# Optimization experiments

Measured on AMD Instinct MI355X. Metric: run time of the kernel, lower is better.

## Reference

```python
import jax, jax.numpy as jnp
import numpy as np

B, T = 64, 512          # batch, input_size
VOCAB = 16              # Embedding(16, ...)
UNITS = 256             # embedding dim
H = 512                 # LSTM hidden units (hard-coded in module)
F = 64                  # num_features (dense output)


def _glorot(key, shape):
    lim = np.sqrt(6.0 / (shape[0] + shape[1]))
    return jax.random.uniform(key, shape, jnp.float32, -lim, lim)


def setup_inputs() -> dict:
    key = jax.random.key(0)
    ks = jax.random.split(key, 9)
    tokens = jax.random.randint(ks[0], (B, T), 0, VOCAB, dtype=jnp.int32)
    return {
        "tokens": tokens,
        "emb": _glorot(ks[1], (VOCAB, UNITS)),
        "W1": _glorot(ks[2], (UNITS, 4 * H)),
        "U1": _glorot(ks[3], (H, 4 * H)),
        "b1": jnp.zeros((4 * H,), jnp.float32),
        "W2": _glorot(ks[4], (H, 4 * H)),
        "U2": _glorot(ks[5], (H, 4 * H)),
        "b2": jnp.zeros((4 * H,), jnp.float32),
        "Wd": _glorot(ks[6], (H, F)),
        "bd": jnp.zeros((F,), jnp.float32),
    }


def _lstm(x, mask, W, U, b, return_sequences):
    # x: [B, T, D]; mask: [B, T] bool. Keras semantics: masked steps carry
    # previous h and c (state and output pass through unchanged).
    xT = jnp.swapaxes(x, 0, 1)      # [T, B, D]
    mT = jnp.swapaxes(mask, 0, 1)   # [T, B]
    h0 = jnp.zeros((x.shape[0], U.shape[0]), x.dtype)
    c0 = h0

    def step(carry, inp):
        h, c = carry
        xt, mt = inp
        z = xt @ W + h @ U + b                    # [B, 4H]
        i, f, g, o = jnp.split(z, 4, axis=-1)     # Keras gate order i,f,c,o
        i = jax.nn.sigmoid(i)
        f = jax.nn.sigmoid(f)
        o = jax.nn.sigmoid(o)
        c_new = f * c + i * jnp.tanh(g)
        h_new = o * jnp.tanh(c_new)
        m = mt[:, None]
        h_new = jnp.where(m, h_new, h)
        c_new = jnp.where(m, c_new, c)
        return (h_new, c_new), h_new

    (h_last, _), hs = jax.lax.scan(step, (h0, c0), (xT, mT))
    return jnp.swapaxes(hs, 0, 1) if return_sequences else h_last


def reference(tokens, emb, W1, U1, b1, W2, U2, b2, Wd, bd):
    mask = tokens != 0                 # mask_zero=True
    x = emb[tokens]                    # [B, T, UNITS]
    h1 = _lstm(x, mask, W1, U1, b1, return_sequences=True)   # [B, T, H]
    h2 = _lstm(h1, mask, W2, U2, b2, return_sequences=False)  # [B, H]
    return h2 @ Wd + bd                # [B, F]
```

## Files before the change

### kernel.cpp

```cpp
#include <hip/hip_runtime.h>

#define BB   64
#define TT   512
#define NVOC 16
#define KIN  256
#define HH   512
#define GG   2048
#define FF   64

#define NWG  256
#define NTHR 512

#define U1W_OFF  0
#define W2W_OFF  8384
#define U2W_OFF  16768
#define HLDS_OFF 25152
#define ZRED_OFF 33344
#define TABW_OFF 37696
#define B2W_OFF  37952
#define LDS_FLOATS 37968
#define LDS_BYTES  (LDS_FLOATS * 4)

#define H1A_OFF 0
#define H1B_OFF 32768
#define H2A_OFF 65536
#define H2B_OFF 98304

__device__ __forceinline__ void wg_barrier(unsigned* ctr, unsigned target) {
  __syncthreads();
  if (threadIdx.x == 0) {
    __hip_atomic_fetch_add(ctr, 1u, __ATOMIC_RELEASE, __HIP_MEMORY_SCOPE_AGENT);
    while (__hip_atomic_load(ctr, __ATOMIC_ACQUIRE, __HIP_MEMORY_SCOPE_AGENT) < target) {
      __builtin_amdgcn_s_sleep(2);
    }
  }
  __syncthreads();
}

__device__ __forceinline__ void stage_ld(float4 v[4], const float* __restrict__ src, int tid) {
  #pragma unroll
  for (int jj = 0; jj < 4; ++jj) {
    int f4 = jj * 512 + tid;
    int b = f4 >> 6, k4l = f4 & 63;
    v[jj] = *reinterpret_cast<const float4*>(src + b * HH + k4l * 4);
  }
}
__device__ __forceinline__ void stage_st(float* __restrict__ hlds, const float4 v[4], int tid) {
  float4* h4 = reinterpret_cast<float4*>(hlds);
  #pragma unroll
  for (int jj = 0; jj < 4; ++jj) {
    int f4 = jj * 512 + tid;
    int b = f4 >> 6, k4l = f4 & 63;
    h4[b * 64 + (k4l ^ (b >> 3))] = v[jj];
  }
}

__device__ __forceinline__ void inner8(float acc[8], const float* __restrict__ wrow,
                                       const float4* __restrict__ h4base, int kq8, int bg) {
  #pragma unroll
  for (int j = 0; j < 8; ++j) {
    int k4 = kq8 + j;
    float4 w = *reinterpret_cast<const float4*>(wrow + k4 * 4);
    const float4* hb = h4base + (k4 ^ bg);
    float4 h0 = hb[0 * 64], h1 = hb[1 * 64], h2 = hb[2 * 64], h3 = hb[3 * 64];
    float4 h4v = hb[4 * 64], h5 = hb[5 * 64], h6 = hb[6 * 64], h7 = hb[7 * 64];
    acc[0] += h0.x * w.x; acc[0] += h0.y * w.y; acc[0] += h0.z * w.z; acc[0] += h0.w * w.w;
    acc[1] += h1.x * w.x; acc[1] += h1.y * w.y; acc[1] += h1.z * w.z; acc[1] += h1.w * w.w;
    acc[2] += h2.x * w.x; acc[2] += h2.y * w.y; acc[2] += h2.z * w.z; acc[2] += h2.w * w.w;
    acc[3] += h3.x * w.x; acc[3] += h3.y * w.y; acc[3] += h3.z * w.z; acc[3] += h3.w * w.w;
    acc[4] += h4v.x * w.x; acc[4] += h4v.y * w.y; acc[4] += h4v.z * w.z; acc[4] += h4v.w * w.w;
    acc[5] += h5.x * w.x; acc[5] += h5.y * w.y; acc[5] += h5.z * w.z; acc[5] += h5.w * w.w;
    acc[6] += h6.x * w.x; acc[6] += h6.y * w.y; acc[6] += h6.z * w.z; acc[6] += h6.w * w.w;
    acc[7] += h7.x * w.x; acc[7] += h7.y * w.y; acc[7] += h7.z * w.z; acc[7] += h7.w * w.w;
  }
}

extern "C" __global__ void __launch_bounds__(NTHR, 2)
lstm_fused2(const int* __restrict__ tokens, const float* __restrict__ emb,
            const float* __restrict__ W1, const float* __restrict__ U1,
            const float* __restrict__ b1, const float* __restrict__ W2,
            const float* __restrict__ U2, const float* __restrict__ b2,
            const float* __restrict__ Wd, const float* __restrict__ bd,
            float* __restrict__ out, float* __restrict__ wsf,
            unsigned* __restrict__ ctr)
{
  extern __shared__ float lds[];
  float* u1w  = lds + U1W_OFF;
  float* w2w  = lds + W2W_OFF;
  float* u2w  = lds + U2W_OFF;
  float* hlds = lds + HLDS_OFF;
  float* zred = lds + ZRED_OFF;
  float* tabw = lds + TABW_OFF;
  float* b2w  = lds + B2W_OFF;

  const int wg  = blockIdx.x;
  const int tid = threadIdx.x;
  const int bh  = wg >> 7;
  const int ct  = wg & 127;
  const int hc0 = ct * 4;
  const int zcl = tid & 15;
  const int bg  = (tid >> 4) & 3;
  const int kq  = tid >> 6;
  const int kq8 = kq * 8;

  float* h1A = wsf + H1A_OFF; float* h1B = wsf + H1B_OFF;
  float* h2A = wsf + H2A_OFF; float* h2B = wsf + H2B_OFF;

  {
    int k = tid;
    #pragma unroll
    for (int g = 0; g < 4; ++g) {
      float4 a = *reinterpret_cast<const float4*>(U1 + (size_t)k * GG + hc0 + 512 * g);
      u1w[(g * 4 + 0) * 524 + k] = a.x; u1w[(g * 4 + 1) * 524 + k] = a.y;
      u1w[(g * 4 + 2) * 524 + k] = a.z; u1w[(g * 4 + 3) * 524 + k] = a.w;
      float4 b_ = *reinterpret_cast<const float4*>(W2 + (size_t)k * GG + hc0 + 512 * g);
      w2w[(g * 4 + 0) * 524 + k] = b_.x; w2w[(g * 4 + 1) * 524 + k] = b_.y;
      w2w[(g * 4 + 2) * 524 + k] = b_.z; w2w[(g * 4 + 3) * 524 + k] = b_.w;
      float4 c_ = *reinterpret_cast<const float4*>(U2 + (size_t)k * GG + hc0 + 512 * g);
      u2w[(g * 4 + 0) * 524 + k] = c_.x; u2w[(g * 4 + 1) * 524 + k] = c_.y;
      u2w[(g * 4 + 2) * 524 + k] = c_.z; u2w[(g * 4 + 3) * 524 + k] = c_.w;
    }
  }
  if (tid < 256) {
    int v = tid >> 4, zz = tid & 15;
    int col = hc0 + (zz & 3) + ((zz >> 2) << 9);
    float a = b1[col];
    #pragma unroll 4
    for (int k = 0; k < KIN; ++k) a += emb[v * KIN + k] * W1[(size_t)k * GG + col];
    tabw[v * 16 + zz] = a;
  }
  if (tid < 16) b2w[tid] = b2[hc0 + (tid & 3) + ((tid >> 2) << 9)];
  {
    if (tid < 128)       h1A[bh * 16384 + ct * 128 + tid] = 0.f;
    else if (tid < 256)  h2A[bh * 16384 + ct * 128 + (tid - 128)] = 0.f;
  }
  unsigned bt = 128;
  wg_barrier(&ctr[bh], bt);

  float c1 = 0.f, hp1 = 0.f, c2 = 0.f, hp2 = 0.f;
  const int fb = tid >> 2;
  const int fc = tid & 3;

  const float4* h4base = reinterpret_cast<const float4*>(hlds) + bg * 512;
  const float* u1row = u1w + zcl * 524;
  const float* w2row = w2w + zcl * 524;
  const float* u2row = u2w + zcl * 524;

  for (int t = 0; t < TT; ++t) {
    float* h1r = (t & 1) ? h1B : h1A;
    float* h1w = (t & 1) ? h1A : h1B;
    float* h2r = (t & 1) ? h2B : h2A;
    float* h2w = (t & 1) ? h2A : h2B;
    const float* h1r_half = h1r + bh * 32 * HH;
    const float* h2r_half = h2r + bh * 32 * HH;
    const float* h1w_half = h1w + bh * 32 * HH;

    float acc[8] = {0,0,0,0,0,0,0,0};
    float4 pre[4];

    stage_ld(pre, h1r_half, tid);
    __syncthreads(); stage_st(hlds, pre, tid); __syncthreads();
    stage_ld(pre, h1r_half + 256, tid);
    inner8(acc, u1row, h4base, kq8, bg);
    __syncthreads(); stage_st(hlds, pre, tid); __syncthreads();
    stage_ld(pre, h2r_half, tid);
    inner8(acc, u1row + 256, h4base, kq8, bg);

    __syncthreads();
    #pragma unroll
    for (int i = 0; i < 8; ++i) zred[kq * 544 + (bg * 8 + i) * 17 + zcl] = acc[i];
    __syncthreads();
    if (tid < 128) {
      float z[4];
      #pragma unroll
      for (int g = 0; g < 4; ++g) {
        float s = 0.f;
        #pragma unroll
        for (int q = 0; q < 8; ++q) s += zred[q * 544 + fb * 17 + g * 4 + fc];
        z[g] = s;
      }
      int tok = tokens[(bh * 32 + fb) * TT + t];
      #pragma unroll
      for (int g = 0; g < 4; ++g) z[g] += tabw[tok * 16 + g * 4 + fc];
      float si = 1.f / (1.f + expf(-z[0]));
      float sf = 1.f / (1.f + expf(-z[1]));
      float gg = tanhf(z[2]);
      float so = 1.f / (1.f + expf(-z[3]));
      float cn = sf * c1 + si * gg;
      float hn = so * tanhf(cn);
      if (tok == 0) { cn = c1; hn = hp1; }
      c1 = cn; hp1 = hn;
      h1w[(bh * 32 + fb) * HH + hc0 + fc] = hn;
    }
    bt += 128; wg_barrier(&ctr[bh], bt);

    #pragma unroll
    for (int i = 0; i < 8; ++i) acc[i] = 0.f;
    __syncthreads(); stage_st(hlds, pre, tid); __syncthreads();
    stage_ld(pre, h2r_half + 256, tid);
    inner8(acc, u2row, h4base, kq8, bg);
    __syncthreads(); stage_st(hlds, pre, tid); __syncthreads();
    stage_ld(pre, h1w_half, tid);
    inner8(acc, u2row + 256, h4base, kq8, bg);
    __syncthreads(); stage_st(hlds, pre, tid); __syncthreads();
    stage_ld(pre, h1w_half + 256, tid);
    inner8(acc, w2row, h4base, kq8, bg);
    __syncthreads(); stage_st(hlds, pre, tid); __syncthreads();
    inner8(acc, w2row + 256, h4base, kq8, bg);

    __syncthreads();
    #pragma unroll
    for (int i = 0; i < 8; ++i) zred[kq * 544 + (bg * 8 + i) * 17 + zcl] = acc[i];
    __syncthreads();
    if (tid < 128) {
      float z[4];
      #pragma unroll
      for (int g = 0; g < 4; ++g) {
        float s = 0.f;
        #pragma unroll
        for (int q = 0; q < 8; ++q) s += zred[q * 544 + fb * 17 + g * 4 + fc];
        z[g] = s + b2w[g * 4 + fc];
      }
      int tok = tokens[(bh * 32 + fb) * TT + t];
      float si = 1.f / (1.f + expf(-z[0]));
      float sf = 1.f / (1.f + expf(-z[1]));
      float gg = tanhf(z[2]);
      float so = 1.f / (1.f + expf(-z[3]));
      float cn = sf * c2 + si * gg;
      float hn = so * tanhf(cn);
      if (tok == 0) { cn = c2; hn = hp2; }
      c2 = cn; hp2 = hn;
      h2w[(bh * 32 + fb) * HH + hc0 + fc] = hn;
    }
    bt += 128; wg_barrier(&ctr[bh], bt);
  }

  if (ct < 4) {
    int idx = ct * 512 + tid;
    int b = idx >> 6, f = idx & 63;
    const float* hf = h2A + (bh * 32 + b) * HH;
    float a = bd[f];
    #pragma unroll 8
    for (int k = 0; k < HH; ++k) a += hf[k] * Wd[(size_t)k * FF + f];
    out[(bh * 32 + b) * FF + f] = a;
  }
}

extern "C" void kernel_launch(void* const* d_in, const int* in_sizes, int n_in,
                              void* d_out, int out_size, void* d_ws, size_t ws_size,
                              hipStream_t stream) {
  const int*   tokens = (const int*)  d_in[0];
  const float* emb    = (const float*)d_in[1];
  const float* W1     = (const float*)d_in[2];
  const float* U1     = (const float*)d_in[3];
  const float* b1     = (const float*)d_in[4];
  const float* W2     = (const float*)d_in[5];
  const float* U2     = (const float*)d_in[6];
  const float* b2     = (const float*)d_in[7];
  const float* Wd     = (const float*)d_in[8];
  const float* bd     = (const float*)d_in[9];
  float*    out = (float*)d_out;
  unsigned* ctr = (unsigned*)d_ws;
  float*    wsf = (float*)((char*)d_ws + 64);

  hipFuncSetAttribute((const void*)lstm_fused2,
                      hipFuncAttributeMaxDynamicSharedMemorySize, LDS_BYTES);

  hipMemsetAsync(d_ws, 0, 64, stream);

  void* args[] = { &tokens, &emb, &W1, &U1, &b1, &W2, &U2, &b2, &Wd, &bd,
                   &out, &wsf, &ctr };
  hipLaunchCooperativeKernel((void*)lstm_fused2, dim3(NWG), dim3(NTHR),
                             args, LDS_BYTES, stream);
}
```

Baseline: 28.02 ms.

## Replace atomic counter barriers with per-workgroup flags and split layer waits

```diff
diff --git a/kernel.cpp b/kernel.cpp
--- a/kernel.cpp
+++ b/kernel.cpp
@@ -21,18 +21,23 @@
 #define LDS_FLOATS 37968
 #define LDS_BYTES  (LDS_FLOATS * 4)
 
+#define FLAG_WORDS 8192
 #define H1A_OFF 0
 #define H1B_OFF 32768
 #define H2A_OFF 65536
 #define H2B_OFF 98304
 
-__device__ __forceinline__ void wg_barrier(unsigned* ctr, unsigned target) {
+__device__ __forceinline__ void bar_arrive(unsigned* flag, unsigned val) {
   __syncthreads();
-  if (threadIdx.x == 0) {
-    __hip_atomic_fetch_add(ctr, 1u, __ATOMIC_RELEASE, __HIP_MEMORY_SCOPE_AGENT);
-    while (__hip_atomic_load(ctr, __ATOMIC_ACQUIRE, __HIP_MEMORY_SCOPE_AGENT) < target) {
-      __builtin_amdgcn_s_sleep(2);
-    }
+  if (threadIdx.x == 0)
+    __hip_atomic_store(flag, val, __ATOMIC_RELEASE, __HIP_MEMORY_SCOPE_AGENT);
+}
+
+__device__ __forceinline__ void bar_wait(unsigned* flags, unsigned target) {
+  if (threadIdx.x < 128) {
+    unsigned* f = flags + threadIdx.x * 16;
+    while (__hip_atomic_load(f, __ATOMIC_ACQUIRE, __HIP_MEMORY_SCOPE_AGENT) < target)
+      __builtin_amdgcn_s_sleep(4);
   }
   __syncthreads();
 }
@@ -76,13 +81,13 @@
 }
 
 extern "C" __global__ void __launch_bounds__(NTHR, 2)
-lstm_fused2(const int* __restrict__ tokens, const float* __restrict__ emb,
+lstm_fused3(const int* __restrict__ tokens, const float* __restrict__ emb,
             const float* __restrict__ W1, const float* __restrict__ U1,
             const float* __restrict__ b1, const float* __restrict__ W2,
             const float* __restrict__ U2, const float* __restrict__ b2,
             const float* __restrict__ Wd, const float* __restrict__ bd,
             float* __restrict__ out, float* __restrict__ wsf,
-            unsigned* __restrict__ ctr)
+            unsigned* __restrict__ flags)
 {
   extern __shared__ float lds[];
   float* u1w  = lds + U1W_OFF;
@@ -102,6 +107,11 @@
   const int bg  = (tid >> 4) & 3;
   const int kq  = tid >> 6;
   const int kq8 = kq * 8;
+
+  unsigned* fA = flags + bh * 2048;
+  unsigned* fB = flags + 4096 + bh * 2048;
+  unsigned* myA = fA + ct * 16;
+  unsigned* myB = fB + ct * 16;
 
   float* h1A = wsf + H1A_OFF; float* h1B = wsf + H1B_OFF;
   float* h2A = wsf + H2A_OFF; float* h2B = wsf + H2B_OFF;
@@ -134,8 +144,9 @@
     if (tid < 128)       h1A[bh * 16384 + ct * 128 + tid] = 0.f;
     else if (tid < 256)  h2A[bh * 16384 + ct * 128 + (tid - 128)] = 0.f;
   }
-  unsigned bt = 128;
-  wg_barrier(&ctr[bh], bt);
+  bar_arrive(myA, 1u);
+  bar_arrive(myB, 1u);
+  bar_wait(fA, 1u);
 
   float c1 = 0.f, hp1 = 0.f, c2 = 0.f, hp2 = 0.f;
   const int fb = tid >> 2;
@@ -154,6 +165,7 @@
     const float* h1r_half = h1r + bh * 32 * HH;
     const float* h2r_half = h2r + bh * 32 * HH;
     const float* h1w_half = h1w + bh * 32 * HH;
+    const unsigned stamp = (unsigned)t + 2u;
 
     float acc[8] = {0,0,0,0,0,0,0,0};
     float4 pre[4];
@@ -163,7 +175,6 @@
     stage_ld(pre, h1r_half + 256, tid);
     inner8(acc, u1row, h4base, kq8, bg);
     __syncthreads(); stage_st(hlds, pre, tid); __syncthreads();
-    stage_ld(pre, h2r_half, tid);
     inner8(acc, u1row + 256, h4base, kq8, bg);
 
     __syncthreads();
@@ -192,16 +203,20 @@
       c1 = cn; hp1 = hn;
       h1w[(bh * 32 + fb) * HH + hc0 + fc] = hn;
     }
-    bt += 128; wg_barrier(&ctr[bh], bt);
-
+    bar_arrive(myA, stamp);
+
+    bar_wait(fB, stamp - 1u);
     #pragma unroll
     for (int i = 0; i < 8; ++i) acc[i] = 0.f;
+    stage_ld(pre, h2r_half, tid);
     __syncthreads(); stage_st(hlds, pre, tid); __syncthreads();
     stage_ld(pre, h2r_half + 256, tid);
     inner8(acc, u2row, h4base, kq8, bg);
     __syncthreads(); stage_st(hlds, pre, tid); __syncthreads();
+    inner8(acc, u2row + 256, h4base, kq8, bg);
+
+    bar_wait(fA, stamp);
     stage_ld(pre, h1w_half, tid);
-    inner8(acc, u2row + 256, h4base, kq8, bg);
     __syncthreads(); stage_st(hlds, pre, tid); __syncthreads();
     stage_ld(pre, h1w_half + 256, tid);
     inner8(acc, w2row, h4base, kq8, bg);
@@ -232,9 +247,10 @@
       c2 = cn; hp2 = hn;
       h2w[(bh * 32 + fb) * HH + hc0 + fc] = hn;
     }
-    bt += 128; wg_barrier(&ctr[bh], bt);
-  }
-
+    bar_arrive(myB, stamp);
+  }
+
+  bar_wait(fB, (unsigned)TT + 1u);
   if (ct < 4) {
     int idx = ct * 512 + tid;
     int b = idx >> 6, f = idx & 63;
@@ -259,17 +275,17 @@
   const float* b2     = (const float*)d_in[7];
   const float* Wd     = (const float*)d_in[8];
   const float* bd     = (const float*)d_in[9];
-  float*    out = (float*)d_out;
-  unsigned* ctr = (unsigned*)d_ws;
-  float*    wsf = (float*)((char*)d_ws + 64);
-
-  hipFuncSetAttribute((const void*)lstm_fused2,
+  float*    out   = (float*)d_out;
+  unsigned* flags = (unsigned*)d_ws;
+  float*    wsf   = (float*)((char*)d_ws + FLAG_WORDS * 4);
+
+  hipFuncSetAttribute((const void*)lstm_fused3,
                       hipFuncAttributeMaxDynamicSharedMemorySize, LDS_BYTES);
 
-  hipMemsetAsync(d_ws, 0, 64, stream);
+  hipMemsetAsync(d_ws, 0, FLAG_WORDS * 4, stream);
 
   void* args[] = { &tokens, &emb, &W1, &U1, &b1, &W2, &U2, &b2, &Wd, &bd,
-                   &out, &wsf, &ctr };
-  hipLaunchCooperativeKernel((void*)lstm_fused2, dim3(NWG), dim3(NTHR),
+                   &out, &wsf, &flags };
+  hipLaunchCooperativeKernel((void*)lstm_fused3, dim3(NWG), dim3(NTHR),
                              args, LDS_BYTES, stream);
 }
```

Measured after the change: 84.17 ms. +200.4%, slower.
